# Performance work log

Measured on AMD Instinct MI355X. Metric: run time of the kernel, lower is better.

## Reference

```python
import math
import jax, jax.numpy as jnp
import numpy as np

# MLA dims (DeepSeek-style, scaled)
B, S, H = 1, 2048, 2048
NH = 16            # num attention heads
DN = 128           # qk_nope_head_dim
DR = 64            # qk_rope_head_dim
DV = 128           # v_head_dim
QL = 1536          # q_lora_rank
KL = 512           # kv_lora_rank
EPS = 1e-6         # rms_norm_eps
ROPE_BASE = 10000.0


def setup_inputs() -> dict:
    key = jax.random.key(0)
    ks = jax.random.split(key, 6)
    w = 0.02  # weight init scale to keep activations sane
    return {
        "hidden": jax.random.normal(ks[0], (B, S, H), jnp.float32),
        "w_kv_a": jax.random.normal(ks[1], (H, QL + KL + DR), jnp.float32) * w,
        "q_a_gamma": jnp.ones((QL,), jnp.float32),
        "w_qb": jax.random.normal(ks[2], (QL, NH * (DN + DR)), jnp.float32) * w,
        "kv_a_gamma": jnp.ones((KL,), jnp.float32),
        "w_kvb": jax.random.normal(ks[3], (KL, NH * (DN + DV)), jnp.float32) * w,
        "w_o": jax.random.normal(ks[4], (NH * DV, H), jnp.float32) * w,
    }


def _rmsnorm(x, gamma, eps=EPS):
    return x * gamma * jax.lax.rsqrt(jnp.mean(x * x, axis=-1, keepdims=True) + eps)


def _rope_tables(seq_len, dim, dtype):
    inv_freq = 1.0 / (ROPE_BASE ** (jnp.arange(0, dim, 2, dtype=jnp.float32) / dim))
    ang = jnp.arange(seq_len, dtype=jnp.float32)[:, None] * inv_freq  # [S, dim/2]
    cos = jnp.concatenate([jnp.cos(ang)] * 2, axis=-1).astype(dtype)  # [S, dim]
    sin = jnp.concatenate([jnp.sin(ang)] * 2, axis=-1).astype(dtype)
    return cos[None, :, None, :], sin[None, :, None, :]  # broadcast to [B,S,h,dim]


def _rotate_half(x):
    h = x.shape[-1] // 2
    return jnp.concatenate([-x[..., h:], x[..., :h]], axis=-1)


def reference(hidden, w_kv_a, q_a_gamma, w_qb, kv_a_gamma, w_kvb, w_o):
    b, s, _ = hidden.shape
    # Fused down-projection: [compressed_q | compressed_kv | k_rope]
    fused = hidden @ w_kv_a                          # [B,S,QL+KL+DR]
    q_c = fused[..., :QL]
    kv_c = fused[..., QL:QL + KL]
    k_pe = fused[..., QL + KL:]                      # [B,S,DR], shared across heads (MQA rope)

    # Q up-projection from normalized latent
    q = _rmsnorm(q_c, q_a_gamma) @ w_qb              # [B,S,NH*(DN+DR)]
    q = q.reshape(b, s, NH, DN + DR)
    q_nope, q_pe = q[..., :DN], q[..., DN:]

    # KV up-projection from normalized latent
    kv = _rmsnorm(kv_c, kv_a_gamma) @ w_kvb          # [B,S,NH*(DN+DV)]
    kv = kv.reshape(b, s, NH, DN + DV)
    k_nope, v = kv[..., :DN], kv[..., DN:]

    # RoPE on the rope slices only
    cos, sin = _rope_tables(s, DR, hidden.dtype)
    q_pe = q_pe * cos + _rotate_half(q_pe) * sin     # [B,S,NH,DR]
    k_pe = k_pe[:, :, None, :]
    k_pe = k_pe * cos + _rotate_half(k_pe) * sin     # [B,S,1,DR]

    q_full = jnp.concatenate([q_nope, q_pe], axis=-1)                         # [B,S,NH,DN+DR]
    k_full = jnp.concatenate([k_nope, jnp.broadcast_to(k_pe, (b, s, NH, DR))], axis=-1)

    scale = 1.0 / math.sqrt(DN + DR)
    scores = jnp.einsum('bqhd,bkhd->bhqk', q_full, k_full) * scale            # [B,NH,S,S]
    pos = jnp.arange(s)
    causal = pos[:, None] >= pos[None, :]
    scores = jnp.where(causal[None, None], scores, jnp.asarray(-1e30, scores.dtype))
    probs = jax.nn.softmax(scores, axis=-1)
    attn = jnp.einsum('bhqk,bkhd->bqhd', probs, v)                            # [B,S,NH,DV]
    return attn.reshape(b, s, NH * DV) @ w_o                                  # [B,S,H]
```

## Files before the change

kernel.cpp:

```cpp
#include <hip/hip_runtime.h>
#include <math.h>

#define S_LEN 2048
#define NH 16
#define DN 128
#define DR 64
#define DV 128
#define QL 1536
#define KL 512
#define FUSED_N 2112
#define FPAD 2176
#define QB_N 3072
#define KVB_N 4096
#define HD_QK 192
#define EPS_RMS 1e-6f

typedef _Float16 f16;
typedef _Float16 half8 __attribute__((ext_vector_type(8)));
typedef _Float16 half4 __attribute__((ext_vector_type(4)));
typedef float floatx4 __attribute__((ext_vector_type(4)));

__global__ __launch_bounds__(256) void cvt_f16_k(const float* __restrict__ in,
                                                 f16* __restrict__ out, int n4)
{
    int i = blockIdx.x * 256 + threadIdx.x;
    if (i < n4) {
        float4 v = ((const float4*)in)[i];
        half4 h;
        h[0] = (f16)v.x; h[1] = (f16)v.y; h[2] = (f16)v.z; h[3] = (f16)v.w;
        ((half4*)out)[i] = h;
    }
}

__global__ __launch_bounds__(256) void tconv_k(const float* __restrict__ in,
                                               f16* __restrict__ out,
                                               int K, int N)
{
    __shared__ float t[32][33];
    const int k0 = blockIdx.y * 32, n0 = blockIdx.x * 32;
    const int c = threadIdx.x & 31, r8 = threadIdx.x >> 5;
    #pragma unroll
    for (int i = 0; i < 4; ++i) {
        int r = r8 + i * 8;
        int gc = n0 + c;
        t[r][c] = (gc < N) ? in[(size_t)(k0 + r) * N + gc] : 0.f;
    }
    __syncthreads();
    #pragma unroll
    for (int i = 0; i < 4; ++i) {
        int r = r8 + i * 8;
        out[(size_t)(n0 + r) * K + k0 + c] = (f16)t[c][r];
    }
}

__device__ __forceinline__ void async16(const f16* gp, f16* lp)
{
    __builtin_amdgcn_global_load_lds(
        (const __attribute__((address_space(1))) void*)gp,
        (__attribute__((address_space(3))) void*)lp, 16, 0, 0);
}

template <int OUT_F16>
__global__ __launch_bounds__(256) void gemm_mfma(
    const f16* __restrict__ A,
    const f16* __restrict__ Bt,
    void* __restrict__ Cv, int M, int N, int K)
{
    __shared__ f16 As[128 * 64];
    __shared__ f16 Bs[128 * 64];

    const int tid = threadIdx.x;
    const int wv = tid >> 6, lane = tid & 63;
    const int quad = lane >> 4, l15 = lane & 15;
    const int wr = wv >> 1, wc = wv & 1;
    const int bm = blockIdx.y * 128, bn = blockIdx.x * 128;
    const int srow = lane >> 3;
    const int sc = lane & 7;

    floatx4 acc[4][4] = {};

    for (int k0 = 0; k0 < K; k0 += 64) {
        #pragma unroll
        for (int t = 0; t < 4; ++t) {
            int rl = wv * 32 + t * 8 + srow;
            int ch = sc ^ (rl & 7);
            async16(A  + (size_t)(bm + rl) * K + k0 + ch * 8,
                    &As[(wv * 32 + t * 8) * 64]);
            async16(Bt + (size_t)(bn + rl) * K + k0 + ch * 8,
                    &Bs[(wv * 32 + t * 8) * 64]);
        }
        __syncthreads();

        #pragma unroll
        for (int ks = 0; ks < 2; ++ks) {
            half8 av[4], bv[4];
            #pragma unroll
            for (int i = 0; i < 4; ++i) {
                int m = wr * 64 + i * 16 + l15;
                av[i] = *(const half8*)&As[m * 64 + ((ks * 4 + quad) ^ (m & 7)) * 8];
            }
            #pragma unroll
            for (int j = 0; j < 4; ++j) {
                int n = wc * 64 + j * 16 + l15;
                bv[j] = *(const half8*)&Bs[n * 64 + ((ks * 4 + quad) ^ (n & 7)) * 8];
            }
            #pragma unroll
            for (int i = 0; i < 4; ++i)
                #pragma unroll
                for (int j = 0; j < 4; ++j)
                    acc[i][j] = __builtin_amdgcn_mfma_f32_16x16x32_f16(
                        av[i], bv[j], acc[i][j], 0, 0, 0);
        }
        __syncthreads();
    }

    #pragma unroll
    for (int i = 0; i < 4; ++i) {
        int rbase = bm + wr * 64 + i * 16 + quad * 4;
        #pragma unroll
        for (int j = 0; j < 4; ++j) {
            int cidx = bn + wc * 64 + j * 16 + l15;
            #pragma unroll
            for (int rr = 0; rr < 4; ++rr) {
                if (OUT_F16)
                    ((f16*)Cv)[(size_t)(rbase + rr) * N + cidx] = (f16)acc[i][j][rr];
                else
                    ((float*)Cv)[(size_t)(rbase + rr) * N + cidx] = acc[i][j][rr];
            }
        }
    }
}

__global__ __launch_bounds__(256) void rmsnorm_k(
    const float* __restrict__ in, int stride, int ncols,
    const float* __restrict__ gamma, f16* __restrict__ out)
{
    const int row = blockIdx.x;
    const float* x = in + (size_t)row * stride;

    float ss = 0.f;
    for (int c = threadIdx.x; c < ncols; c += 256) {
        float v = x[c];
        ss += v * v;
    }
    #pragma unroll
    for (int off = 32; off > 0; off >>= 1) ss += __shfl_down(ss, off);

    __shared__ float warp_s[4];
    __shared__ float scale_s;
    const int wid = threadIdx.x >> 6;
    if ((threadIdx.x & 63) == 0) warp_s[wid] = ss;
    __syncthreads();
    if (threadIdx.x == 0) {
        float t = warp_s[0] + warp_s[1] + warp_s[2] + warp_s[3];
        scale_s = rsqrtf(t / (float)ncols + EPS_RMS);
    }
    __syncthreads();
    const float sc = scale_s;
    for (int c = threadIdx.x; c < ncols; c += 256)
        out[(size_t)row * ncols + c] = (f16)(x[c] * gamma[c] * sc);
}

__device__ __forceinline__ float rope_one(int s, int d, float x, float other)
{
    const int j = d & 31;
    const float invf = expf(-0.28782313662425572f * (float)j);
    const float ang = (float)s * invf;
    float sn, cs;
    sincosf(ang, &sn, &cs);
    float rot = (d < 32) ? -other : other;
    return x * cs + rot * sn;
}

__global__ __launch_bounds__(256) void rope_q_k(f16* __restrict__ q)
{
    const int s = blockIdx.x;
    const int h = blockIdx.y * 4 + (threadIdx.x >> 6);
    const int d = threadIdx.x & 63;
    f16* base = q + (size_t)s * QB_N + h * HD_QK + DN;
    float x = (float)base[d];
    float other = (float)((d < 32) ? base[d + 32] : base[d - 32]);
    base[d] = (f16)rope_one(s, d, x, other);
}

__global__ __launch_bounds__(256) void kfull_k(const f16* __restrict__ kv,
                                               const float* __restrict__ fused,
                                               f16* __restrict__ kfull)
{
    int n = blockIdx.x * 256 + threadIdx.x;
    int c8 = n % 24;
    int s = (n / 24) & 2047;
    int h = n / (24 * 2048);
    half8 v;
    if (c8 < 16) {
        v = *(const half8*)&kv[(size_t)s * KVB_N + h * 256 + c8 * 8];
    } else {
        const float* src = fused + (size_t)s * FPAD + (QL + KL);
        int dbase = (c8 - 16) * 8;
        #pragma unroll
        for (int j = 0; j < 8; ++j) {
            int d = dbase + j;
            float x = src[d];
            float other = src[(d < 32) ? d + 32 : d - 32];
            v[j] = (f16)rope_one(s, d, x, other);
        }
    }
    *(half8*)&kfull[((size_t)h * S_LEN + s) * HD_QK + c8 * 8] = v;
}

__global__ __launch_bounds__(256) void vt_k(const f16* __restrict__ kv,
                                            f16* __restrict__ vt)
{
    __shared__ f16 t[32][33];
    const int s0 = blockIdx.x * 32, d0 = blockIdx.y * 32, h = blockIdx.z;
    const int tid = threadIdx.x;
    {
        const int c = tid & 31, rb = tid >> 5;
        #pragma unroll
        for (int i = 0; i < 4; ++i) {
            int r = rb + i * 8;
            t[r][c] = kv[(size_t)(s0 + r) * KVB_N + h * 256 + 128 + d0 + c];
        }
    }
    __syncthreads();
    {
        const int d = tid >> 3, s4 = tid & 7;
        half4 v;
        v[0] = t[s4 * 4 + 0][d];
        v[1] = t[s4 * 4 + 1][d];
        v[2] = t[s4 * 4 + 2][d];
        v[3] = t[s4 * 4 + 3][d];
        *(half4*)&vt[((size_t)h * DV + d0 + d) * S_LEN + s0 + s4 * 4] = v;
    }
}

__global__ __launch_bounds__(256) void attn_mfma_k(
    const f16* __restrict__ q,
    const f16* __restrict__ kfull,
    const f16* __restrict__ vt,
    f16* __restrict__ part_o,
    float* __restrict__ part_ml)
{
    __shared__ f16 sm[25088];

    const int tid = threadIdx.x;
    const int w = tid >> 6, lane = tid & 63;
    const int quad = lane >> 4, l15 = lane & 15;
    const int wbase = w * 64;
    const int h = blockIdx.y;
    const int z = blockIdx.z;
    const int qb = (blockIdx.y < 8) ? (int)blockIdx.x : 31 - (int)blockIdx.x;
    const int q0 = qb * 64;
    const int kt_begin = z ? (qb + 1) : 0;
    const int kt_end   = z ? (2 * qb + 2) : (qb + 1);
    const float scale2 = 0.10411755f;

    const f16* kf_h = kfull + (size_t)h * S_LEN * HD_QK;
    const f16* vt_h = vt + (size_t)h * DV * S_LEN;

    int koff[3];
    #pragma unroll
    for (int j = 0; j < 3; ++j) {
        int sig = j * 256 + tid;
        int r = sig / 24, cs = sig - r * 24;
        int ch = (cs & 24) | ((cs & 7) ^ (r & 7));
        koff[j] = r * HD_QK + ch * 8;
    }
    int voff[2];
    #pragma unroll
    for (int j = 0; j < 2; ++j) {
        int sig = j * 256 + tid;
        int rv = sig >> 2, c = (sig & 3) ^ ((rv >> 1) & 3);
        voff[j] = rv * S_LEN + c * 8;
    }

    #pragma unroll
    for (int j = 0; j < 6; ++j) {
        int sig = j * 256 + tid;
        int r = sig / 24, cs = sig - r * 24;
        int ch = (cs & 24) | ((cs & 7) ^ (r & 7));
        async16(q + (size_t)(q0 + r) * QB_N + h * HD_QK + ch * 8,
                sm + 10240 + (j * 256 + wbase) * 8);
    }
    {
        const f16* kg = kf_h + (size_t)kt_begin * 32 * HD_QK;
        const f16* vg = vt_h + kt_begin * 32;
        #pragma unroll
        for (int j = 0; j < 3; ++j) async16(kg + koff[j], sm + (j * 256 + wbase) * 8);
        #pragma unroll
        for (int j = 0; j < 2; ++j) async16(vg + voff[j], sm + 6144 + (j * 256 + wbase) * 8);
    }
    __syncthreads();

    half8 qf[6];
    const int qrow = w * 16 + l15;
    #pragma unroll
    for (int kd = 0; kd < 6; ++kd) {
        int c = kd * 4 + quad;
        int cs = (c & 24) | ((c & 7) ^ (qrow & 7));
        qf[kd] = *(const half8*)&sm[10240 + (qrow * 24 + cs) * 8];
    }

    half8 ones_h;
    #pragma unroll
    for (int j = 0; j < 8; ++j) ones_h[j] = (f16)1.0f;

    floatx4 o[8] = {};
    floatx4 o_l = {};
    float m_i[4];
    #pragma unroll
    for (int r = 0; r < 4; ++r) m_i[r] = -1e30f;

    const int qrow_min = q0 + w * 16;
    f16* Pw = sm + 22528 + w * 640;

    for (int kt = kt_begin; kt < kt_end; ++kt) {
        const int cur = (kt - kt_begin) & 1;
        __syncthreads();
        if (kt + 1 < kt_end) {
            const int nxt = 1 - cur;
            const int k0n = (kt + 1) * 32;
            f16* kb = sm + (nxt ? 10240 : 0);
            f16* vb = sm + (nxt ? 16384 : 6144);
            const f16* kg = kf_h + (size_t)k0n * HD_QK;
            const f16* vg = vt_h + k0n;
            #pragma unroll
            for (int j = 0; j < 3; ++j) async16(kg + koff[j], kb + (j * 256 + wbase) * 8);
            #pragma unroll
            for (int j = 0; j < 2; ++j) async16(vg + voff[j], vb + (j * 256 + wbase) * 8);
        }
        const int k0 = kt * 32;
        if (k0 > qrow_min + 15) continue;

        const f16* kb = sm + (cur ? 10240 : 0);
        const f16* vb = sm + (cur ? 16384 : 6144);

        floatx4 s0 = {}, s1 = {};
        #pragma unroll
        for (int kd = 0; kd < 6; ++kd) {
            int c = kd * 4 + quad;
            int cs = (c & 24) | ((c & 7) ^ (l15 & 7));
            half8 b0 = *(const half8*)&kb[(l15 * 24 + cs) * 8];
            half8 b1 = *(const half8*)&kb[((l15 + 16) * 24 + cs) * 8];
            s0 = __builtin_amdgcn_mfma_f32_16x16x32_f16(qf[kd], b0, s0, 0, 0, 0);
            s1 = __builtin_amdgcn_mfma_f32_16x16x32_f16(qf[kd], b1, s1, 0, 0, 0);
        }

        const bool nm = (k0 + 31 > qrow_min);
        float mt[4];
        #pragma unroll
        for (int r = 0; r < 4; ++r) {
            float v0 = s0[r] * scale2, v1 = s1[r] * scale2;
            if (nm) {
                int row = qrow_min + quad * 4 + r;
                if (k0 + l15 > row)      v0 = -1e30f;
                if (k0 + 16 + l15 > row) v1 = -1e30f;
            }
            s0[r] = v0; s1[r] = v1;
            mt[r] = fmaxf(v0, v1);
        }
        #pragma unroll
        for (int r = 0; r < 4; ++r) {
            mt[r] = fmaxf(mt[r], __shfl_xor(mt[r], 1));
            mt[r] = fmaxf(mt[r], __shfl_xor(mt[r], 2));
            mt[r] = fmaxf(mt[r], __shfl_xor(mt[r], 4));
            mt[r] = fmaxf(mt[r], __shfl_xor(mt[r], 8));
        }
        float alpha[4];
        #pragma unroll
        for (int r = 0; r < 4; ++r) {
            float mn = fmaxf(m_i[r], mt[r]);
            alpha[r] = __builtin_exp2f(m_i[r] - mn);
            m_i[r] = mn;
            s0[r] = __builtin_exp2f(s0[r] - mn);
            s1[r] = __builtin_exp2f(s1[r] - mn);
        }

        #pragma unroll
        for (int r = 0; r < 4; ++r) {
            Pw[(quad * 4 + r) * 40 + l15]      = (f16)s0[r];
            Pw[(quad * 4 + r) * 40 + 16 + l15] = (f16)s1[r];
        }

        #pragma unroll
        for (int nb = 0; nb < 8; ++nb)
            #pragma unroll
            for (int r = 0; r < 4; ++r) o[nb][r] *= alpha[r];
        #pragma unroll
        for (int r = 0; r < 4; ++r) o_l[r] *= alpha[r];

        half8 pa = *(const half8*)&Pw[l15 * 40 + quad * 8];
        o_l = __builtin_amdgcn_mfma_f32_16x16x32_f16(pa, ones_h, o_l, 0, 0, 0);
        #pragma unroll
        for (int nb = 0; nb < 8; ++nb) {
            int rv = nb * 16 + l15;
            int sig = rv * 4 + (quad ^ ((l15 >> 1) & 3));
            half8 vv = *(const half8*)&vb[sig * 8];
            o[nb] = __builtin_amdgcn_mfma_f32_16x16x32_f16(pa, vv, o[nb], 0, 0, 0);
        }
    }

    float inv[4];
    #pragma unroll
    for (int r = 0; r < 4; ++r) inv[r] = (o_l[r] > 0.f) ? 1.f / o_l[r] : 0.f;

    f16* po = part_o + (size_t)z * S_LEN * 2048;
    #pragma unroll
    for (int nb = 0; nb < 8; ++nb) {
        #pragma unroll
        for (int r = 0; r < 4; ++r) {
            int row = q0 + w * 16 + quad * 4 + r;
            po[(size_t)row * (NH * DV) + h * DV + nb * 16 + l15] =
                (f16)(o[nb][r] * inv[r]);
        }
    }
    if (l15 == 0) {
        #pragma unroll
        for (int r = 0; r < 4; ++r) {
            int row = q0 + w * 16 + quad * 4 + r;
            float* ml = part_ml + (((size_t)z * NH + h) * S_LEN + row) * 2;
            ml[0] = m_i[r];
            ml[1] = o_l[r];
        }
    }
}

__global__ __launch_bounds__(256) void attn_comb_k(
    const f16* __restrict__ part_o, const float* __restrict__ part_ml,
    f16* __restrict__ attnb)
{
    int g = blockIdx.x * 256 + threadIdx.x;
    int h = (g >> 4) & 15;
    int s = g >> 8;
    const float* ml0 = part_ml + ((size_t)h * S_LEN + s) * 2;
    const float* ml1 = part_ml + (((size_t)NH + h) * S_LEN + s) * 2;
    float m0 = ml0[0], l0 = ml0[1];
    float m1 = ml1[0], l1 = ml1[1];
    float M = fmaxf(m0, m1);
    float w0 = l0 * __builtin_exp2f(m0 - M);
    float w1 = l1 * __builtin_exp2f(m1 - M);
    float inv = 1.f / (w0 + w1);
    w0 *= inv; w1 *= inv;
    half8 p0 = *(const half8*)&part_o[(size_t)g * 8];
    half8 p1 = *(const half8*)&part_o[(size_t)(524288 + g) * 8];
    half8 r;
    #pragma unroll
    for (int j = 0; j < 8; ++j)
        r[j] = (f16)(w0 * (float)p0[j] + w1 * (float)p1[j]);
    *(half8*)&attnb[(size_t)g * 8] = r;
}

extern "C" void kernel_launch(void* const* d_in, const int* in_sizes, int n_in,
                              void* d_out, int out_size, void* d_ws, size_t ws_size,
                              hipStream_t stream)
{
    const float* hidden   = (const float*)d_in[0];
    const float* w_kv_a   = (const float*)d_in[1];
    const float* q_gamma  = (const float*)d_in[2];
    const float* w_qb     = (const float*)d_in[3];
    const float* kv_gamma = (const float*)d_in[4];
    const float* w_kvb    = (const float*)d_in[5];
    const float* w_o      = (const float*)d_in[6];
    float* out = (float*)d_out;

    char* p = (char*)d_ws;
    f16* hid_h   = (f16*)p;  p += (size_t)2048 * 2048 * 2;
    f16* wkva_t  = (f16*)p;  p += (size_t)2176 * 2048 * 2;
    f16* wqb_t   = (f16*)p;  p += (size_t)3072 * 1536 * 2;
    f16* wkvb_t  = (f16*)p;  p += (size_t)4096 * 512 * 2;
    f16* wo_t    = (f16*)p;  p += (size_t)2048 * 2048 * 2;
    float* fused = (float*)p; p += (size_t)2048 * FPAD * 4;
    f16* q_n     = (f16*)p;  p += (size_t)2048 * QL * 2;
    f16* qbuf    = (f16*)p;  p += (size_t)2048 * QB_N * 2;
    f16* kv_n    = (f16*)p;  p += (size_t)2048 * KL * 2;
    f16* kvbuf   = (f16*)p;  p += (size_t)2048 * KVB_N * 2;
    f16* attnb   = (f16*)p;  p += (size_t)2048 * 2048 * 2;
    f16* part_o  = (f16*)p;  p += (size_t)2 * 2048 * 2048 * 2;
    float* part_ml = (float*)p; p += (size_t)2 * NH * 2048 * 2 * 4;

    f16* kfull = hid_h;
    f16* vt    = (f16*)fused;

    dim3 blk(256);

    cvt_f16_k<<<(2048 * 2048 / 4 + 255) / 256, blk, 0, stream>>>(hidden, hid_h, 2048 * 2048 / 4);
    tconv_k<<<dim3(2176 / 32, 2048 / 32), blk, 0, stream>>>(w_kv_a, wkva_t, 2048, FUSED_N);
    tconv_k<<<dim3(3072 / 32, 1536 / 32), blk, 0, stream>>>(w_qb,   wqb_t,  1536, QB_N);
    tconv_k<<<dim3(4096 / 32,  512 / 32), blk, 0, stream>>>(w_kvb,  wkvb_t,  512, KVB_N);
    tconv_k<<<dim3(2048 / 32, 2048 / 32), blk, 0, stream>>>(w_o,    wo_t,   2048, 2048);

    gemm_mfma<0><<<dim3(FPAD / 128, 2048 / 128), blk, 0, stream>>>(
        hid_h, wkva_t, fused, 2048, FPAD, 2048);

    rmsnorm_k<<<2048, blk, 0, stream>>>(fused, FPAD, QL, q_gamma, q_n);
    rmsnorm_k<<<2048, blk, 0, stream>>>(fused + QL, FPAD, KL, kv_gamma, kv_n);

    gemm_mfma<1><<<dim3(QB_N / 128, 2048 / 128), blk, 0, stream>>>(
        q_n, wqb_t, qbuf, 2048, QB_N, QL);
    gemm_mfma<1><<<dim3(KVB_N / 128, 2048 / 128), blk, 0, stream>>>(
        kv_n, wkvb_t, kvbuf, 2048, KVB_N, KL);

    rope_q_k<<<dim3(2048, 4), blk, 0, stream>>>(qbuf);

    kfull_k<<<16 * 2048 * 24 / 256, blk, 0, stream>>>(kvbuf, fused, kfull);
    vt_k<<<dim3(2048 / 32, 128 / 32, NH), blk, 0, stream>>>(kvbuf, vt);

    attn_mfma_k<<<dim3(32, NH, 2), blk, 0, stream>>>(qbuf, kfull, vt, part_o, part_ml);
    attn_comb_k<<<2048, blk, 0, stream>>>(part_o, part_ml, attnb);

    gemm_mfma<0><<<dim3(2048 / 128, 2048 / 128), blk, 0, stream>>>(
        attnb, wo_t, out, 2048, 2048, 2048);
}
```

Measured before the change: 391.8 us.

## Double-buffer LDS tiles in MFMA GEMM to overlap global loads with compute

The GEMM kernel now keeps two LDS buffers for the A and B tiles. It issues the async global-to-LDS loads for the next K step before running the MFMAs on the current one, and uses one barrier per iteration instead of two. Per-thread global offsets are precomputed outside the loop. The aim is to hide global load latency behind matrix math, at the cost of doubling LDS use per block, which may reduce occupancy.

New measurement: 356.6 us. 9.0% less time.

```diff
diff --git a/kernel.cpp b/kernel.cpp
--- a/kernel.cpp
+++ b/kernel.cpp
@@ -66,8 +66,7 @@
     const f16* __restrict__ Bt,
     void* __restrict__ Cv, int M, int N, int K)
 {
-    __shared__ f16 As[128 * 64];
-    __shared__ f16 Bs[128 * 64];
+    __shared__ f16 sm[2][2][128 * 64];
 
     const int tid = threadIdx.x;
     const int wv = tid >> 6, lane = tid & 63;
@@ -77,19 +76,41 @@
     const int srow = lane >> 3;
     const int sc = lane & 7;
 
+    size_t aoff[4], boff[4];
+    int ldst[4];
+    #pragma unroll
+    for (int t = 0; t < 4; ++t) {
+        int rl = wv * 32 + t * 8 + srow;
+        int ch = sc ^ (rl & 7);
+        aoff[t] = (size_t)(bm + rl) * K + ch * 8;
+        boff[t] = (size_t)(bn + rl) * K + ch * 8;
+        ldst[t] = (wv * 32 + t * 8) * 64;
+    }
+
+    #pragma unroll
+    for (int t = 0; t < 4; ++t) {
+        async16(A  + aoff[t], &sm[0][0][ldst[t]]);
+        async16(Bt + boff[t], &sm[0][1][ldst[t]]);
+    }
+
     floatx4 acc[4][4] = {};
-
-    for (int k0 = 0; k0 < K; k0 += 64) {
-        #pragma unroll
-        for (int t = 0; t < 4; ++t) {
-            int rl = wv * 32 + t * 8 + srow;
-            int ch = sc ^ (rl & 7);
-            async16(A  + (size_t)(bm + rl) * K + k0 + ch * 8,
-                    &As[(wv * 32 + t * 8) * 64]);
-            async16(Bt + (size_t)(bn + rl) * K + k0 + ch * 8,
-                    &Bs[(wv * 32 + t * 8) * 64]);
-        }
+    const int nsteps = K >> 6;
+
+    for (int step = 0; step < nsteps; ++step) {
+        const int cur = step & 1;
         __syncthreads();
+        if (step + 1 < nsteps) {
+            const int k0n = (step + 1) << 6;
+            f16* Ab = sm[1 - cur][0];
+            f16* Bb = sm[1 - cur][1];
+            #pragma unroll
+            for (int t = 0; t < 4; ++t) {
+                async16(A  + aoff[t] + k0n, Ab + ldst[t]);
+                async16(Bt + boff[t] + k0n, Bb + ldst[t]);
+            }
+        }
+        const f16* As = sm[cur][0];
+        const f16* Bs = sm[cur][1];
 
         #pragma unroll
         for (int ks = 0; ks < 2; ++ks) {
@@ -111,7 +132,6 @@
                     acc[i][j] = __builtin_amdgcn_mfma_f32_16x16x32_f16(
                         av[i], bv[j], acc[i][j], 0, 0, 0);
         }
-        __syncthreads();
     }
 
     #pragma unroll
```
